# Kernel tuning notes

Measured on AMD Instinct MI355X. Metric: run time of the kernel, lower is better.

Reference implementation:

```python
import jax, jax.numpy as jnp
import numpy as np
from jax import lax

B, C, H, W = 2, 64, 128, 128
F_SCALE, STRIDE = 2, 2
F = F_SCALE * STRIDE            # pixel-unshuffle factor = 4
CK = C // 16                    # attention channel dim = 4
SCALE_DIM = C // F_SCALE        # softmax scale uses embed_size//f_scale = 32


def setup_inputs() -> dict:
    key = jax.random.key(0)
    ks = jax.random.split(key, 16)
    g = lambda i, shape, s=0.05: jax.random.normal(ks[i], shape, jnp.float32) * s
    return {
        "x":   jax.random.normal(ks[0], (B, C, H, W), jnp.float32),
        # conv1 = Sequential(1x1 C->CK, 1x1 CK->CK)
        "w1a": g(1, (CK, C)), "b1a": g(2, (CK,)),
        "w1b": g(3, (CK, CK)), "b1b": g(4, (CK,)),
        # wqk parameter (torch.randn, std 1)
        "wqk": jax.random.normal(ks[5], (CK, CK), jnp.float32),
        # conv2: 1x1 CK->C ; conv: 1x1 C->C
        "w2":  g(6, (C, CK)), "b2": g(7, (C,)),
        "wc":  g(8, (C, C)), "bc": g(9, (C,)),
        # FF (GridSANaive): 1x1 C->C/4, 3x3 dilated C/4->C/4, 1x1 C/4->C
        "wf1": g(10, (C // 4, C)), "bf1": g(11, (C // 4,)),
        "wf2": g(12, (C // 4, C // 4, 3, 3)), "bf2": g(13, (C // 4,)),
        "wf3": g(14, (C, C // 4)), "bf3": g(15, (C,)),
    }


def conv1x1(x, w, b):
    return jnp.einsum('bchw,oc->bohw', x, w) + b[None, :, None, None]


def grid_attention(x, wqk):
    b, c, h, w = x.shape
    sh = h // 2
    x = jnp.pad(x, ((0, 0), (0, 0), (sh, 0), (0, 0)))      # Shift2d pad (top)
    # F.layer_norm over last 3 dims, no affine, eps=1e-5
    mu = jnp.mean(x, axis=(1, 2, 3), keepdims=True)
    var = jnp.var(x, axis=(1, 2, 3), keepdims=True)
    xx = (x - mu) / jnp.sqrt(var + 1e-5)
    hh, ww = xx.shape[2], xx.shape[3]
    ph, pw = (F - hh % F) % F, (F - ww % F) % F
    xx = jnp.pad(xx, ((0, 0), (0, 0), (0, ph), (0, pw)))
    gh, gw = (hh + ph) // F, (ww + pw) // F
    # pixel_unshuffle: channel layout (c, fy, fx)
    xx = xx.reshape(b, c, gh, F, gw, F).transpose(0, 1, 3, 5, 2, 4)
    xx = xx.reshape(b, c * F * F, gh, gw)
    # rearrange 'b (f c) h w -> (b f) c h w', f=F*F (mixes layout, as in original)
    xx = xx.reshape(b * F * F, c, gh, gw)
    L = gh * gw
    tok = xx.transpose(0, 2, 3, 1).reshape(b * F * F, L, c)   # (bg, L, c)
    qk = tok @ wqk
    qk = qk / (jnp.linalg.norm(qk, axis=-1, keepdims=True) + 1e-8)
    attn = (jnp.einsum('blk,bmk->blm', qk, qk) + 1.0) / (SCALE_DIM ** 0.5)
    attn = jax.nn.softmax(attn, axis=-1)
    out = jnp.einsum('blm,bmc->blc', attn, tok)
    out = out.reshape(b * F * F, gh, gw, c).transpose(0, 3, 1, 2)
    out = out.reshape(b, F * F * c, gh, gw)
    # pixel_shuffle: channel layout (fy, fx, c)
    out = out.reshape(b, F, F, c, gh, gw).transpose(0, 3, 4, 1, 5, 2)
    out = out.reshape(b, c, gh * F, gw * F)
    out = out[:, :, :hh, :ww]                               # undo shuffle pad
    return out[:, :, :-sh, :] if sh > 0 else out            # Shift2d crop (bottom)


def ff(x, wf1, bf1, wf2, bf2, wf3, bf3):
    h1 = jax.nn.relu(conv1x1(x, wf1, bf1))
    k = 1 + (STRIDE // 2) * 2   # ShiftConv2d offset for 3x3, dilation=STRIDE
    hp = jnp.pad(h1, ((0, 0), (0, 0), (k, 0), (0, 0)))
    h2 = lax.conv_general_dilated(
        hp, wf2, (1, 1), ((STRIDE, STRIDE), (STRIDE, STRIDE)),
        rhs_dilation=(STRIDE, STRIDE),
        dimension_numbers=('NCHW', 'OIHW', 'NCHW'))
    h2 = jax.nn.relu((h2 + bf2[None, :, None, None])[:, :, :-k, :])
    return conv1x1(h2, wf3, bf3)


def reference(x, w1a, b1a, w1b, b1b, wqk, w2, b2, wc, bc,
              wf1, bf1, wf2, bf2, wf3, bf3):
    a = conv1x1(conv1x1(x, w1a, b1a), w1b, b1b)
    att = grid_attention(a, wqk)
    y = x + conv1x1(conv1x1(att, w2, b2), wc, bc)
    return y + ff(y, wf1, bf1, wf2, bf2, wf3, bf3)
```

## Files before the change

### kernel.cpp

```cpp
#include <hip/hip_runtime.h>
#include <math.h>

#define CHW  (64*16384)
#define ATT_SCALE 0.17677669529663687f

__global__ __launch_bounds__(256) void k1_a_stats(
    const float* __restrict__ x, const float* __restrict__ w1a,
    const float* __restrict__ b1a, const float* __restrict__ w1b,
    const float* __restrict__ b1b, float* __restrict__ a,
    float* __restrict__ statsbuf) {
  __shared__ float sA[256];
  __shared__ float sb1[4];
  __shared__ float4 part[8][32][4];
  __shared__ float rs[128], rq[128];
  int tid = threadIdx.x;
  {
    int o = tid >> 6, c = tid & 63;
    float s = 0.f;
    #pragma unroll
    for (int k = 0; k < 4; ++k) s += w1b[o*4+k] * w1a[k*64+c];
    sA[tid] = s;
  }
  if (tid < 4) {
    float s = b1b[tid];
    #pragma unroll
    for (int k = 0; k < 4; ++k) s += w1b[tid*4+k] * b1a[k];
    sb1[tid] = s;
  }
  __syncthreads();
  int quad = tid & 31, cg = tid >> 5;
  int gq = blockIdx.x * 32 + quad;
  int bb = gq >> 12;
  int px0 = (gq & 4095) * 4;
  const float* xp = x + bb*CHW + (cg*8)*16384 + px0;
  float4 acc[4];
  #pragma unroll
  for (int o = 0; o < 4; ++o) acc[o] = make_float4(0.f,0.f,0.f,0.f);
  #pragma unroll
  for (int cc = 0; cc < 8; ++cc) {
    float4 xv = *(const float4*)(xp + cc*16384);
    int c = cg*8 + cc;
    #pragma unroll
    for (int o = 0; o < 4; ++o) {
      float w = sA[o*64+c];
      acc[o].x += w*xv.x; acc[o].y += w*xv.y; acc[o].z += w*xv.z; acc[o].w += w*xv.w;
    }
  }
  #pragma unroll
  for (int o = 0; o < 4; ++o) part[cg][quad][o] = acc[o];
  __syncthreads();
  float ls = 0.f, lq = 0.f;
  if (tid < 128) {
    int q2 = tid & 31, o = tid >> 5;
    float4 s = part[0][q2][o];
    #pragma unroll
    for (int g2 = 1; g2 < 8; ++g2) {
      float4 p = part[g2][q2][o];
      s.x += p.x; s.y += p.y; s.z += p.z; s.w += p.w;
    }
    float bv = sb1[o];
    s.x += bv; s.y += bv; s.z += bv; s.w += bv;
    int gq2 = blockIdx.x*32 + q2;
    int b2 = gq2 >> 12; int p0 = (gq2 & 4095)*4;
    *(float4*)(a + b2*4*16384 + o*16384 + p0) = s;
    ls = s.x+s.y+s.z+s.w;
    lq = s.x*s.x+s.y*s.y+s.z*s.z+s.w*s.w;
    rs[tid] = ls; rq[tid] = lq;
  }
  __syncthreads();
  for (int s2 = 64; s2; s2 >>= 1) {
    if (tid < s2) { rs[tid] += rs[tid+s2]; rq[tid] += rq[tid+s2]; }
    __syncthreads();
  }
  if (tid == 0) { statsbuf[blockIdx.x*2] = rs[0]; statsbuf[blockIdx.x*2+1] = rq[0]; }
}

__global__ __launch_bounds__(256) void k2_tok_qk(
    const float* __restrict__ a, const float* __restrict__ statsbuf,
    const float* __restrict__ wqk, float4* __restrict__ tok,
    float4* __restrict__ qko) {
  __shared__ float rs[128], rq[128];
  int tid = threadIdx.x;
  int g = blockIdx.x / 6;
  int t = (blockIdx.x % 6) * 256 + tid;
  int b = g >> 4, u = (g >> 2) & 3, v = g & 3;
  if (tid < 128) {
    rs[tid] = statsbuf[(b*128+tid)*2];
    rq[tid] = statsbuf[(b*128+tid)*2+1];
  }
  __syncthreads();
  for (int s2 = 64; s2; s2 >>= 1) {
    if (tid < s2) { rs[tid] += rs[tid+s2]; rq[tid] += rq[tid+s2]; }
    __syncthreads();
  }
  float mu  = rs[0] * (1.f/98304.f);
  float var = rq[0] * (1.f/98304.f) - mu*mu;
  float rsig = rsqrtf(var + 1e-5f);
  int i = t >> 5, j = t & 31;
  int Hp = i*4 + v;
  float4 tv;
  if (Hp >= 64) {
    tv = *(const float4*)(a + (b*4+u)*16384 + (Hp-64)*128 + j*4);
    tv.x = (tv.x-mu)*rsig; tv.y = (tv.y-mu)*rsig;
    tv.z = (tv.z-mu)*rsig; tv.w = (tv.w-mu)*rsig;
  } else {
    float z = -mu*rsig;
    tv = make_float4(z,z,z,z);
  }
  float q0 = tv.x*wqk[0] + tv.y*wqk[4] + tv.z*wqk[8]  + tv.w*wqk[12];
  float q1 = tv.x*wqk[1] + tv.y*wqk[5] + tv.z*wqk[9]  + tv.w*wqk[13];
  float q2 = tv.x*wqk[2] + tv.y*wqk[6] + tv.z*wqk[10] + tv.w*wqk[14];
  float q3 = tv.x*wqk[3] + tv.y*wqk[7] + tv.z*wqk[11] + tv.w*wqk[15];
  float nrm = sqrtf(q0*q0 + q1*q1 + q2*q2 + q3*q3);
  float inv = 1.f / (nrm + 1e-8f);
  int idx = g*1536 + t;
  tok[idx] = tv;
  qko[idx] = make_float4(q0*inv, q1*inv, q2*inv, q3*inv);
}

__device__ __forceinline__ float poly_exp(float d) {
  return 1.f + d*(1.f + d*(0.5f + d*(0.16666667f + d*0.04166667f)));
}
__global__ __launch_bounds__(256) void k3_attn(
    const float4* __restrict__ tok, const float4* __restrict__ qk,
    float* __restrict__ att) {
  __shared__ float4 kq[1024];
  __shared__ float4 kt[1024];
  __shared__ float red[128][8][5];
  int tid = threadIdx.x;
  int g = blockIdx.x >> 3, qb = blockIdx.x & 7;
  const float4* qg = qk  + g*1536;
  const float4* tg = tok + g*1536;
  for (int m = tid; m < 1024; m += 256) { kq[m] = qg[512+m]; kt[m] = tg[512+m]; }
  __syncthreads();
  int s = tid >> 5, qi = tid & 31;
  int t0 = qb*128 + qi*4;
  float4 q[4];
  #pragma unroll
  for (int j = 0; j < 4; ++j) {
    float4 v = qg[t0+j];
    q[j] = make_float4(v.x*ATT_SCALE, v.y*ATT_SCALE, v.z*ATT_SCALE, v.w*ATT_SCALE);
  }
  float den[4] = {0.f,0.f,0.f,0.f};
  float4 ov[4];
  #pragma unroll
  for (int j = 0; j < 4; ++j) ov[j] = make_float4(0.f,0.f,0.f,0.f);
  if (s == 0) {
    float4 k0 = qg[0]; float4 tv0 = tg[0];
    #pragma unroll
    for (int j = 0; j < 4; ++j) {
      float d = q[j].x*k0.x + q[j].y*k0.y + q[j].z*k0.z + q[j].w*k0.w;
      float e = 512.f * poly_exp(d);
      den[j] += e;
      ov[j].x += e*tv0.x; ov[j].y += e*tv0.y; ov[j].z += e*tv0.z; ov[j].w += e*tv0.w;
    }
  }
  int m0 = s * 128;
  #pragma unroll 2
  for (int m = m0; m < m0 + 128; ++m) {
    float4 kk = kq[m];
    float4 tv = kt[m];
    #pragma unroll
    for (int j = 0; j < 4; ++j) {
      float d = q[j].x*kk.x + q[j].y*kk.y + q[j].z*kk.z + q[j].w*kk.w;
      float e = poly_exp(d);
      den[j] += e;
      ov[j].x += e*tv.x; ov[j].y += e*tv.y; ov[j].z += e*tv.z; ov[j].w += e*tv.w;
    }
  }
  #pragma unroll
  for (int j = 0; j < 4; ++j) {
    red[qi*4+j][s][0] = den[j];
    red[qi*4+j][s][1] = ov[j].x; red[qi*4+j][s][2] = ov[j].y;
    red[qi*4+j][s][3] = ov[j].z; red[qi*4+j][s][4] = ov[j].w;
  }
  __syncthreads();
  if (tid < 128) {
    float dsum=0.f, ox=0.f, oy=0.f, oz=0.f, ow=0.f;
    #pragma unroll
    for (int ss = 0; ss < 8; ++ss) {
      dsum += red[tid][ss][0];
      ox += red[tid][ss][1]; oy += red[tid][ss][2];
      oz += red[tid][ss][3]; ow += red[tid][ss][4];
    }
    float inv = 1.f / dsum;
    int t = qb*128 + tid;
    int b = g >> 4, u = (g >> 2) & 3, v = g & 3;
    int i = t >> 5, j = t & 31;
    float* ap = att + b*4*16384 + (i*4+u)*128 + (j*4+v);
    ap[0]     = ox*inv;
    ap[16384] = oy*inv;
    ap[32768] = oz*inv;
    ap[49152] = ow*inv;
  }
}

__global__ __launch_bounds__(256) void k4_y_h1(
    const float* __restrict__ x, const float* __restrict__ att,
    const float* __restrict__ w2p, const float* __restrict__ b2p,
    const float* __restrict__ wcp, const float* __restrict__ bcp,
    const float* __restrict__ wf1, const float* __restrict__ bf1,
    float* __restrict__ yout, float* __restrict__ h1) {
  __shared__ float sWf[64][4];
  __shared__ float sbf[64];
  __shared__ float sw1[1024];
  __shared__ float sb1[16];
  __shared__ float4 satt[4][32];
  __shared__ float4 ylds[64][32];
  int tid = threadIdx.x;
  {
    int o = tid >> 2, k = tid & 3;
    float s = 0.f;
    for (int c = 0; c < 64; ++c) s += wcp[o*64+c] * w2p[c*4+k];
    sWf[o][k] = s;
  }
  if (tid < 64) {
    float s = bcp[tid];
    for (int c = 0; c < 64; ++c) s += wcp[tid*64+c] * b2p[c];
    sbf[tid] = s;
  }
  for (int i = tid; i < 1024; i += 256) sw1[i] = wf1[i];
  if (tid < 16) sb1[tid] = bf1[tid];
  int quad = tid & 31, og = tid >> 5;
  int gq = blockIdx.x*32 + quad;
  int bb = gq >> 12; int px0 = (gq & 4095)*4;
  if (tid < 128) {
    int k = tid >> 5, q2 = tid & 31;
    int gq2 = blockIdx.x*32 + q2;
    int b2i = gq2 >> 12; int p0 = (gq2 & 4095)*4;
    satt[k][q2] = *(const float4*)(att + b2i*4*16384 + k*16384 + p0);
  }
  __syncthreads();
  float4 a0 = satt[0][quad], a1 = satt[1][quad], a2 = satt[2][quad], a3 = satt[3][quad];
  const float* xp = x + bb*CHW + px0;
  float* yp = yout + bb*CHW + px0;
  #pragma unroll
  for (int cc = 0; cc < 8; ++cc) {
    int c = og*8 + cc;
    float4 xv = *(const float4*)(xp + c*16384);
    float w0 = sWf[c][0], w1 = sWf[c][1], w2v = sWf[c][2], w3 = sWf[c][3];
    float bv = sbf[c];
    float4 yv;
    yv.x = xv.x + w0*a0.x + w1*a1.x + w2v*a2.x + w3*a3.x + bv;
    yv.y = xv.y + w0*a0.y + w1*a1.y + w2v*a2.y + w3*a3.y + bv;
    yv.z = xv.z + w0*a0.z + w1*a1.z + w2v*a2.z + w3*a3.z + bv;
    yv.w = xv.w + w0*a0.w + w1*a1.w + w2v*a2.w + w3*a3.w + bv;
    *(float4*)(yp + c*16384) = yv;
    ylds[c][quad] = yv;
  }
  __syncthreads();
  int o2a = og*2, o2b = og*2+1;
  float4 acc0 = make_float4(sb1[o2a], sb1[o2a], sb1[o2a], sb1[o2a]);
  float4 acc1 = make_float4(sb1[o2b], sb1[o2b], sb1[o2b], sb1[o2b]);
  #pragma unroll 8
  for (int c = 0; c < 64; ++c) {
    float4 yv = ylds[c][quad];
    float wa = sw1[o2a*64+c], wb = sw1[o2b*64+c];
    acc0.x += wa*yv.x; acc0.y += wa*yv.y; acc0.z += wa*yv.z; acc0.w += wa*yv.w;
    acc1.x += wb*yv.x; acc1.y += wb*yv.y; acc1.z += wb*yv.z; acc1.w += wb*yv.w;
  }
  acc0.x = fmaxf(acc0.x,0.f); acc0.y = fmaxf(acc0.y,0.f);
  acc0.z = fmaxf(acc0.z,0.f); acc0.w = fmaxf(acc0.w,0.f);
  acc1.x = fmaxf(acc1.x,0.f); acc1.y = fmaxf(acc1.y,0.f);
  acc1.z = fmaxf(acc1.z,0.f); acc1.w = fmaxf(acc1.w,0.f);
  float* hp = h1 + bb*16*16384 + px0;
  *(float4*)(hp + o2a*16384) = acc0;
  *(float4*)(hp + o2b*16384) = acc1;
}

__global__ __launch_bounds__(256) void k6_ff_out(
    const float* __restrict__ h1, const float* __restrict__ wf2,
    const float* __restrict__ bf2, const float* __restrict__ wf3,
    const float* __restrict__ bf3, float* yo) {
  __shared__ float sbuf[16][3][136];
  __shared__ float h2buf[128][21];
  int tid = threadIdx.x;
  int bb = blockIdx.x >> 7, h = blockIdx.x & 127;
  for (int idx = tid; idx < 16*3*136; idx += 256) {
    int c = idx / (3*136);
    int r = (idx / 136) % 3;
    int col = idx % 136;
    int row = h - 5 + 2*r;
    int w = col - 4;
    float v = 0.f;
    if (row >= 0 && w >= 0 && w < 128)
      v = h1[bb*16*16384 + c*16384 + row*128 + w];
    sbuf[c][r][col] = v;
  }
  __syncthreads();
  int w = tid & 127;
  int g = __builtin_amdgcn_readfirstlane(tid >> 7);
  float acc[8];
  #pragma unroll
  for (int o = 0; o < 8; ++o) acc[o] = bf2[g*8+o];
  #pragma unroll 4
  for (int c = 0; c < 16; ++c) {
    #pragma unroll
    for (int r = 0; r < 3; ++r) {
      float tm2 = sbuf[c][r][w+2];
      float t00 = sbuf[c][r][w+4];
      float tp2 = sbuf[c][r][w+6];
      #pragma unroll
      for (int o = 0; o < 8; ++o) {
        const float* wp = wf2 + (((g*8+o)*16 + c)*3 + r)*3;
        acc[o] += wp[0]*tm2 + wp[1]*t00 + wp[2]*tp2;
      }
    }
  }
  #pragma unroll
  for (int o = 0; o < 8; ++o) h2buf[w][g*8+o] = fmaxf(acc[o], 0.f);
  __syncthreads();
  float hv[16];
  #pragma unroll
  for (int k = 0; k < 16; ++k) hv[k] = h2buf[w][k];
  float* ybase = yo + bb*CHW + h*128 + w;
  #pragma unroll 4
  for (int oc = 0; oc < 32; ++oc) {
    int o = g*32 + oc;
    float sv = bf3[o] + ybase[o*16384];
    #pragma unroll
    for (int k = 0; k < 16; ++k) sv += wf3[o*16+k]*hv[k];
    ybase[o*16384] = sv;
  }
}

extern "C" void kernel_launch(void* const* d_in, const int* in_sizes, int n_in,
                              void* d_out, int out_size, void* d_ws, size_t ws_size,
                              hipStream_t stream) {
  (void)in_sizes; (void)n_in; (void)out_size; (void)ws_size;
  const float* x   = (const float*)d_in[0];
  const float* w1a = (const float*)d_in[1];
  const float* b1a = (const float*)d_in[2];
  const float* w1b = (const float*)d_in[3];
  const float* b1b = (const float*)d_in[4];
  const float* wqk = (const float*)d_in[5];
  const float* w2  = (const float*)d_in[6];
  const float* b2  = (const float*)d_in[7];
  const float* wc  = (const float*)d_in[8];
  const float* bc  = (const float*)d_in[9];
  const float* wf1 = (const float*)d_in[10];
  const float* bf1 = (const float*)d_in[11];
  const float* wf2 = (const float*)d_in[12];
  const float* bf2 = (const float*)d_in[13];
  const float* wf3 = (const float*)d_in[14];
  const float* bf3 = (const float*)d_in[15];

  float* ws = (float*)d_ws;
  float*  a_    = ws;
  float*  stats = ws + 131072;
  float4* tok   = (float4*)(ws + 131584);
  float4* qkb   = (float4*)(ws + 328192);
  float*  att   = ws + 524800;
  float*  h1    = ws + 655872;
  float*  y     = (float*)d_out;

  k1_a_stats<<<256, 256, 0, stream>>>(x, w1a, b1a, w1b, b1b, a_, stats);
  k2_tok_qk <<<192, 256, 0, stream>>>(a_, stats, wqk, tok, qkb);
  k3_attn   <<<256, 256, 0, stream>>>(tok, qkb, att);
  k4_y_h1   <<<256, 256, 0, stream>>>(x, att, w2, b2, wc, bc, wf1, bf1, y, h1);
  k6_ff_out <<<256, 256, 0, stream>>>(h1, wf2, bf2, wf3, bf3, y);
}
```

Before: 156.2 us.

## Double thread-level parallelism across stats, attention and FF kernels

Splits work across more threads in every kernel. k1 runs 512 blocks with 16 channel groups of 4, k3/k4/k6 run 512-thread blocks with half the per-thread work (16 key slices, one h1 output channel, 4 conv outputs per thread). Shared-memory reduction buffers are relaid out to be conflict-free and the stats/workspace offsets are adjusted. The aim is more waves in flight on a 256-CU GPU to hide latency, at the cost of bigger cross-thread reductions and more registers per block.

```diff
diff --git a/kernel.cpp b/kernel.cpp
--- a/kernel.cpp
+++ b/kernel.cpp
@@ -11,8 +11,8 @@
     float* __restrict__ statsbuf) {
   __shared__ float sA[256];
   __shared__ float sb1[4];
-  __shared__ float4 part[8][32][4];
-  __shared__ float rs[128], rq[128];
+  __shared__ float pc[4][4][256];
+  __shared__ float rs[64], rq[64];
   int tid = threadIdx.x;
   {
     int o = tid >> 6, c = tid & 63;
@@ -28,18 +28,18 @@
     sb1[tid] = s;
   }
   __syncthreads();
-  int quad = tid & 31, cg = tid >> 5;
-  int gq = blockIdx.x * 32 + quad;
+  int quad = tid & 15, cg = tid >> 4;
+  int gq = blockIdx.x * 16 + quad;
   int bb = gq >> 12;
   int px0 = (gq & 4095) * 4;
-  const float* xp = x + bb*CHW + (cg*8)*16384 + px0;
+  const float* xp = x + bb*CHW + (cg*4)*16384 + px0;
   float4 acc[4];
   #pragma unroll
   for (int o = 0; o < 4; ++o) acc[o] = make_float4(0.f,0.f,0.f,0.f);
   #pragma unroll
-  for (int cc = 0; cc < 8; ++cc) {
+  for (int cc = 0; cc < 4; ++cc) {
     float4 xv = *(const float4*)(xp + cc*16384);
-    int c = cg*8 + cc;
+    int c = cg*4 + cc;
     #pragma unroll
     for (int o = 0; o < 4; ++o) {
       float w = sA[o*64+c];
@@ -47,28 +47,30 @@
     }
   }
   #pragma unroll
-  for (int o = 0; o < 4; ++o) part[cg][quad][o] = acc[o];
-  __syncthreads();
-  float ls = 0.f, lq = 0.f;
-  if (tid < 128) {
-    int q2 = tid & 31, o = tid >> 5;
-    float4 s = part[0][q2][o];
-    #pragma unroll
-    for (int g2 = 1; g2 < 8; ++g2) {
-      float4 p = part[g2][q2][o];
-      s.x += p.x; s.y += p.y; s.z += p.z; s.w += p.w;
+  for (int o = 0; o < 4; ++o) {
+    pc[0][o][tid] = acc[o].x; pc[1][o][tid] = acc[o].y;
+    pc[2][o][tid] = acc[o].z; pc[3][o][tid] = acc[o].w;
+  }
+  __syncthreads();
+  if (tid < 64) {
+    int q2 = tid & 15, o = tid >> 4;
+    float sx=0.f, sy=0.f, sz=0.f, sw=0.f;
+    #pragma unroll
+    for (int g2 = 0; g2 < 16; ++g2) {
+      int idx = g2*16 + q2;
+      sx += pc[0][o][idx]; sy += pc[1][o][idx];
+      sz += pc[2][o][idx]; sw += pc[3][o][idx];
     }
     float bv = sb1[o];
-    s.x += bv; s.y += bv; s.z += bv; s.w += bv;
-    int gq2 = blockIdx.x*32 + q2;
+    sx += bv; sy += bv; sz += bv; sw += bv;
+    int gq2 = blockIdx.x*16 + q2;
     int b2 = gq2 >> 12; int p0 = (gq2 & 4095)*4;
-    *(float4*)(a + b2*4*16384 + o*16384 + p0) = s;
-    ls = s.x+s.y+s.z+s.w;
-    lq = s.x*s.x+s.y*s.y+s.z*s.z+s.w*s.w;
-    rs[tid] = ls; rq[tid] = lq;
-  }
-  __syncthreads();
-  for (int s2 = 64; s2; s2 >>= 1) {
+    *(float4*)(a + b2*4*16384 + o*16384 + p0) = make_float4(sx,sy,sz,sw);
+    rs[tid] = sx+sy+sz+sw;
+    rq[tid] = sx*sx+sy*sy+sz*sz+sw*sw;
+  }
+  __syncthreads();
+  for (int s2 = 32; s2; s2 >>= 1) {
     if (tid < s2) { rs[tid] += rs[tid+s2]; rq[tid] += rq[tid+s2]; }
     __syncthreads();
   }
@@ -79,17 +81,15 @@
     const float* __restrict__ a, const float* __restrict__ statsbuf,
     const float* __restrict__ wqk, float4* __restrict__ tok,
     float4* __restrict__ qko) {
-  __shared__ float rs[128], rq[128];
+  __shared__ float rs[256], rq[256];
   int tid = threadIdx.x;
   int g = blockIdx.x / 6;
   int t = (blockIdx.x % 6) * 256 + tid;
   int b = g >> 4, u = (g >> 2) & 3, v = g & 3;
-  if (tid < 128) {
-    rs[tid] = statsbuf[(b*128+tid)*2];
-    rq[tid] = statsbuf[(b*128+tid)*2+1];
-  }
-  __syncthreads();
-  for (int s2 = 64; s2; s2 >>= 1) {
+  rs[tid] = statsbuf[(b*256+tid)*2];
+  rq[tid] = statsbuf[(b*256+tid)*2+1];
+  __syncthreads();
+  for (int s2 = 128; s2; s2 >>= 1) {
     if (tid < s2) { rs[tid] += rs[tid+s2]; rq[tid] += rq[tid+s2]; }
     __syncthreads();
   }
@@ -121,19 +121,19 @@
 __device__ __forceinline__ float poly_exp(float d) {
   return 1.f + d*(1.f + d*(0.5f + d*(0.16666667f + d*0.04166667f)));
 }
-__global__ __launch_bounds__(256) void k3_attn(
+__global__ __launch_bounds__(512) void k3_attn(
     const float4* __restrict__ tok, const float4* __restrict__ qk,
     float* __restrict__ att) {
   __shared__ float4 kq[1024];
   __shared__ float4 kt[1024];
-  __shared__ float red[128][8][5];
+  __shared__ float red[16][5][128];
   int tid = threadIdx.x;
   int g = blockIdx.x >> 3, qb = blockIdx.x & 7;
   const float4* qg = qk  + g*1536;
   const float4* tg = tok + g*1536;
-  for (int m = tid; m < 1024; m += 256) { kq[m] = qg[512+m]; kt[m] = tg[512+m]; }
-  __syncthreads();
-  int s = tid >> 5, qi = tid & 31;
+  for (int m = tid; m < 1024; m += 512) { kq[m] = qg[512+m]; kt[m] = tg[512+m]; }
+  __syncthreads();
+  int qi = tid & 31, s = tid >> 5;
   int t0 = qb*128 + qi*4;
   float4 q[4];
   #pragma unroll
@@ -155,9 +155,9 @@
       ov[j].x += e*tv0.x; ov[j].y += e*tv0.y; ov[j].z += e*tv0.z; ov[j].w += e*tv0.w;
     }
   }
-  int m0 = s * 128;
+  int m0 = s * 64;
   #pragma unroll 2
-  for (int m = m0; m < m0 + 128; ++m) {
+  for (int m = m0; m < m0 + 64; ++m) {
     float4 kk = kq[m];
     float4 tv = kt[m];
     #pragma unroll
@@ -170,21 +170,23 @@
   }
   #pragma unroll
   for (int j = 0; j < 4; ++j) {
-    red[qi*4+j][s][0] = den[j];
-    red[qi*4+j][s][1] = ov[j].x; red[qi*4+j][s][2] = ov[j].y;
-    red[qi*4+j][s][3] = ov[j].z; red[qi*4+j][s][4] = ov[j].w;
+    int key = j*32 + qi;
+    red[s][0][key] = den[j];
+    red[s][1][key] = ov[j].x; red[s][2][key] = ov[j].y;
+    red[s][3][key] = ov[j].z; red[s][4][key] = ov[j].w;
   }
   __syncthreads();
   if (tid < 128) {
+    int qi_r = tid & 31, j_r = tid >> 5;
     float dsum=0.f, ox=0.f, oy=0.f, oz=0.f, ow=0.f;
     #pragma unroll
-    for (int ss = 0; ss < 8; ++ss) {
-      dsum += red[tid][ss][0];
-      ox += red[tid][ss][1]; oy += red[tid][ss][2];
-      oz += red[tid][ss][3]; ow += red[tid][ss][4];
+    for (int ss = 0; ss < 16; ++ss) {
+      dsum += red[ss][0][tid];
+      ox += red[ss][1][tid]; oy += red[ss][2][tid];
+      oz += red[ss][3][tid]; ow += red[ss][4][tid];
     }
     float inv = 1.f / dsum;
-    int t = qb*128 + tid;
+    int t = qb*128 + qi_r*4 + j_r;
     int b = g >> 4, u = (g >> 2) & 3, v = g & 3;
     int i = t >> 5, j = t & 31;
     float* ap = att + b*4*16384 + (i*4+u)*128 + (j*4+v);
@@ -195,7 +197,7 @@
   }
 }
 
-__global__ __launch_bounds__(256) void k4_y_h1(
+__global__ __launch_bounds__(512) void k4_y_h1(
     const float* __restrict__ x, const float* __restrict__ att,
     const float* __restrict__ w2p, const float* __restrict__ b2p,
     const float* __restrict__ wcp, const float* __restrict__ bcp,
@@ -208,7 +210,7 @@
   __shared__ float4 satt[4][32];
   __shared__ float4 ylds[64][32];
   int tid = threadIdx.x;
-  {
+  if (tid < 256) {
     int o = tid >> 2, k = tid & 3;
     float s = 0.f;
     for (int c = 0; c < 64; ++c) s += wcp[o*64+c] * w2p[c*4+k];
@@ -219,7 +221,7 @@
     for (int c = 0; c < 64; ++c) s += wcp[tid*64+c] * b2p[c];
     sbf[tid] = s;
   }
-  for (int i = tid; i < 1024; i += 256) sw1[i] = wf1[i];
+  for (int i = tid; i < 1024; i += 512) sw1[i] = wf1[i];
   if (tid < 16) sb1[tid] = bf1[tid];
   int quad = tid & 31, og = tid >> 5;
   int gq = blockIdx.x*32 + quad;
@@ -235,8 +237,8 @@
   const float* xp = x + bb*CHW + px0;
   float* yp = yout + bb*CHW + px0;
   #pragma unroll
-  for (int cc = 0; cc < 8; ++cc) {
-    int c = og*8 + cc;
+  for (int cc = 0; cc < 4; ++cc) {
+    int c = og*4 + cc;
     float4 xv = *(const float4*)(xp + c*16384);
     float w0 = sWf[c][0], w1 = sWf[c][1], w2v = sWf[c][2], w3 = sWf[c][3];
     float bv = sbf[c];
@@ -249,26 +251,20 @@
     ylds[c][quad] = yv;
   }
   __syncthreads();
-  int o2a = og*2, o2b = og*2+1;
-  float4 acc0 = make_float4(sb1[o2a], sb1[o2a], sb1[o2a], sb1[o2a]);
-  float4 acc1 = make_float4(sb1[o2b], sb1[o2b], sb1[o2b], sb1[o2b]);
+  float bv = sb1[og];
+  float4 acc = make_float4(bv, bv, bv, bv);
   #pragma unroll 8
   for (int c = 0; c < 64; ++c) {
     float4 yv = ylds[c][quad];
-    float wa = sw1[o2a*64+c], wb = sw1[o2b*64+c];
-    acc0.x += wa*yv.x; acc0.y += wa*yv.y; acc0.z += wa*yv.z; acc0.w += wa*yv.w;
-    acc1.x += wb*yv.x; acc1.y += wb*yv.y; acc1.z += wb*yv.z; acc1.w += wb*yv.w;
-  }
-  acc0.x = fmaxf(acc0.x,0.f); acc0.y = fmaxf(acc0.y,0.f);
-  acc0.z = fmaxf(acc0.z,0.f); acc0.w = fmaxf(acc0.w,0.f);
-  acc1.x = fmaxf(acc1.x,0.f); acc1.y = fmaxf(acc1.y,0.f);
-  acc1.z = fmaxf(acc1.z,0.f); acc1.w = fmaxf(acc1.w,0.f);
-  float* hp = h1 + bb*16*16384 + px0;
-  *(float4*)(hp + o2a*16384) = acc0;
-  *(float4*)(hp + o2b*16384) = acc1;
-}
-
-__global__ __launch_bounds__(256) void k6_ff_out(
+    float wa = sw1[og*64+c];
+    acc.x += wa*yv.x; acc.y += wa*yv.y; acc.z += wa*yv.z; acc.w += wa*yv.w;
+  }
+  acc.x = fmaxf(acc.x,0.f); acc.y = fmaxf(acc.y,0.f);
+  acc.z = fmaxf(acc.z,0.f); acc.w = fmaxf(acc.w,0.f);
+  *(float4*)(h1 + bb*16*16384 + og*16384 + px0) = acc;
+}
+
+__global__ __launch_bounds__(512) void k6_ff_out(
     const float* __restrict__ h1, const float* __restrict__ wf2,
     const float* __restrict__ bf2, const float* __restrict__ wf3,
     const float* __restrict__ bf3, float* yo) {
@@ -276,7 +272,7 @@
   __shared__ float h2buf[128][21];
   int tid = threadIdx.x;
   int bb = blockIdx.x >> 7, h = blockIdx.x & 127;
-  for (int idx = tid; idx < 16*3*136; idx += 256) {
+  for (int idx = tid; idx < 16*3*136; idx += 512) {
     int c = idx / (3*136);
     int r = (idx / 136) % 3;
     int col = idx % 136;
@@ -290,9 +286,9 @@
   __syncthreads();
   int w = tid & 127;
   int g = __builtin_amdgcn_readfirstlane(tid >> 7);
-  float acc[8];
-  #pragma unroll
-  for (int o = 0; o < 8; ++o) acc[o] = bf2[g*8+o];
+  float acc[4];
+  #pragma unroll
+  for (int o = 0; o < 4; ++o) acc[o] = bf2[g*4+o];
   #pragma unroll 4
   for (int c = 0; c < 16; ++c) {
     #pragma unroll
@@ -301,22 +297,22 @@
       float t00 = sbuf[c][r][w+4];
       float tp2 = sbuf[c][r][w+6];
       #pragma unroll
-      for (int o = 0; o < 8; ++o) {
-        const float* wp = wf2 + (((g*8+o)*16 + c)*3 + r)*3;
+      for (int o = 0; o < 4; ++o) {
+        const float* wp = wf2 + (((g*4+o)*16 + c)*3 + r)*3;
         acc[o] += wp[0]*tm2 + wp[1]*t00 + wp[2]*tp2;
       }
     }
   }
   #pragma unroll
-  for (int o = 0; o < 8; ++o) h2buf[w][g*8+o] = fmaxf(acc[o], 0.f);
+  for (int o = 0; o < 4; ++o) h2buf[w][g*4+o] = fmaxf(acc[o], 0.f);
   __syncthreads();
   float hv[16];
   #pragma unroll
   for (int k = 0; k < 16; ++k) hv[k] = h2buf[w][k];
   float* ybase = yo + bb*CHW + h*128 + w;
   #pragma unroll 4
-  for (int oc = 0; oc < 32; ++oc) {
-    int o = g*32 + oc;
+  for (int oc = 0; oc < 16; ++oc) {
+    int o = g*16 + oc;
     float sv = bf3[o] + ybase[o*16384];
     #pragma unroll
     for (int k = 0; k < 16; ++k) sv += wf3[o*16+k]*hv[k];
@@ -348,15 +344,15 @@
   float* ws = (float*)d_ws;
   float*  a_    = ws;
   float*  stats = ws + 131072;
-  float4* tok   = (float4*)(ws + 131584);
-  float4* qkb   = (float4*)(ws + 328192);
-  float*  att   = ws + 524800;
-  float*  h1    = ws + 655872;
+  float4* tok   = (float4*)(ws + 132096);
+  float4* qkb   = (float4*)(ws + 328704);
+  float*  att   = ws + 525312;
+  float*  h1    = ws + 656384;
   float*  y     = (float*)d_out;
 
-  k1_a_stats<<<256, 256, 0, stream>>>(x, w1a, b1a, w1b, b1b, a_, stats);
+  k1_a_stats<<<512, 256, 0, stream>>>(x, w1a, b1a, w1b, b1b, a_, stats);
   k2_tok_qk <<<192, 256, 0, stream>>>(a_, stats, wqk, tok, qkb);
-  k3_attn   <<<256, 256, 0, stream>>>(tok, qkb, att);
-  k4_y_h1   <<<256, 256, 0, stream>>>(x, att, w2, b2, wc, bc, wf1, bf1, y, h1);
-  k6_ff_out <<<256, 256, 0, stream>>>(h1, wf2, bf2, wf3, bf3, y);
-}
+  k3_attn   <<<256, 512, 0, stream>>>(tok, qkb, att);
+  k4_y_h1   <<<256, 512, 0, stream>>>(x, att, w2, b2, wc, bc, wf1, bf1, y, h1);
+  k6_ff_out <<<256, 512, 0, stream>>>(h1, wf2, bf2, wf3, bf3, y);
+}
```

After: 134.1 us. 14.1% less time.
